# Performance work log

Hardware: AMD Instinct MI355X
Metric: run time of the kernel (lower is better)

## Reference

```python
import jax, jax.numpy as jnp
import numpy as np

TANH_SCALAR = 10.0  # taug in IrEne eq. 1 (close_to_one setting)

N_NODES = 2**21 - 1   # complete binary tree, depth D=21
N_LEAVES = 2**20
NUM_FEATURES = 64


def setup_inputs() -> dict:
    key = jax.random.key(0)
    k1, k2, k3, k4 = jax.random.split(key, 4)
    features = jax.random.normal(k1, (N_NODES, NUM_FEATURES), dtype=jnp.float32)
    leaf_energy = jax.random.uniform(k2, (N_LEAVES,), dtype=jnp.float32)
    W = jax.random.normal(k3, (NUM_FEATURES, 1), dtype=jnp.float32) * 0.1
    b = jax.random.normal(k4, (1,), dtype=jnp.float32) * 0.1
    return {"features": features, "leaf_energy": leaf_energy, "W": W, "b": b}


def reference(features, leaf_energy, W, b):
    """Batched equivalent of RecursiveTreeComputation (close_to_one, end2end).

    Tree layout: complete binary tree in level order; node i's parent is (i-1)//2.
    Level d occupies indices [2^d - 1, 2^{d+1} - 1). Leaves are the last level.
    parent_energy = sum_children score(child) * child_energy,
    score(f) = 1 + tanh(f @ W + b) / tanh_scalar.
    Returns predicted energy for every node, shape [N].
    """
    N, F = features.shape
    D = int(np.log2(N + 1))  # number of levels (static)

    # One fused pass over all nodes: Linear(F,1) + tanh + affine (WeightingModel).
    scores = 1.0 + jnp.tanh(features @ W + b)[:, 0] / TANH_SCALAR  # [N]

    leaf_start = 2 ** (D - 1) - 1
    energy = jnp.zeros((N,), dtype=features.dtype).at[leaf_start:].set(leaf_energy)

    # Level-wise bottom-up accumulation; consecutive child pairs share a parent.
    for d in range(D - 1, 0, -1):
        start, end = 2 ** d - 1, 2 ** (d + 1) - 1          # children at level d
        contrib = scores[start:end] * energy[start:end]      # weighted child energies
        parent_vals = contrib.reshape(-1, 2).sum(axis=1)     # sum sibling pairs
        pstart = 2 ** (d - 1) - 1                             # parents at level d-1
        energy = energy.at[pstart:start].set(energy[pstart:start] + parent_vals)
    return energy
```

## Files before the change

### kernel.cpp

```cpp
#include <hip/hip_runtime.h>
#include <cmath>

#define N_NODES_C   ((1 << 21) - 1)
#define N_LEAVES_C  (1 << 20)
#define LEAF_START  (N_LEAVES_C - 1)
#define NFEAT       64

__device__ __forceinline__ float score_fn(float dot, float bias) {
    return 1.0f + tanhf(dot + bias) * 0.1f;
}

__global__ __launch_bounds__(256) void scores_kernel(
        const float* __restrict__ features,
        const float* __restrict__ W,
        const float* __restrict__ b,
        float* __restrict__ scores) {
    const int q = threadIdx.x & 15;
    const float4 w4 = ((const float4*)W)[q];
    const float bias = b[0];
    const int group0 = (blockIdx.x * 256 + threadIdx.x) >> 4;
    const int stride = (gridDim.x * 256) >> 4;
    for (int node = group0; node < N_NODES_C; node += stride) {
        const float4 f = ((const float4*)(features + (size_t)node * NFEAT))[q];
        float v = f.x * w4.x + f.y * w4.y + f.z * w4.z + f.w * w4.w;
        v += __shfl_xor(v, 1);
        v += __shfl_xor(v, 2);
        v += __shfl_xor(v, 4);
        v += __shfl_xor(v, 8);
        if (q == 0) scores[node] = score_fn(v, bias);
    }
}

__global__ __launch_bounds__(256) void stage1_kernel(
        const float* __restrict__ scores,
        const float* __restrict__ leaf_energy,
        float* __restrict__ out) {
    __shared__ float buf[2][4096];
    const int blk = blockIdx.x;
    const int tid = threadIdx.x;
    const int leaf_off = blk * 4096;

    for (int i = tid; i < 4096; i += 256) {
        const int g = LEAF_START + leaf_off + i;
        const float e = leaf_energy[leaf_off + i];
        out[g] = e;
        buf[0][i] = scores[g] * e;
    }
    __syncthreads();

    int p = 0;
    for (int pd = 19; pd >= 8; --pd) {
        const int m = 1 << (pd - 8);
        const int base = (1 << pd) - 1 + blk * m;
        for (int j = tid; j < m; j += 256) {
            const float val = buf[p][2 * j] + buf[p][2 * j + 1];
            out[base + j] = val;
            buf[1 - p][j] = scores[base + j] * val;
        }
        p ^= 1;
        __syncthreads();
    }
}

__global__ __launch_bounds__(256) void stage2_kernel(
        const float* __restrict__ scores,
        float* __restrict__ out) {
    __shared__ float buf[2][256];
    const int tid = threadIdx.x;
    buf[0][tid] = scores[255 + tid] * out[255 + tid];
    __syncthreads();
    int p = 0;
    for (int pd = 7; pd >= 0; --pd) {
        const int m = 1 << pd;
        const int base = m - 1;
        if (tid < m) {
            const float val = buf[p][2 * tid] + buf[p][2 * tid + 1];
            out[base + tid] = val;
            buf[1 - p][tid] = scores[base + tid] * val;
        }
        p ^= 1;
        __syncthreads();
    }
}

extern "C" void kernel_launch(void* const* d_in, const int* in_sizes, int n_in,
                              void* d_out, int out_size, void* d_ws, size_t ws_size,
                              hipStream_t stream) {
    const float* features    = (const float*)d_in[0];
    const float* leaf_energy = (const float*)d_in[1];
    const float* W           = (const float*)d_in[2];
    const float* b           = (const float*)d_in[3];
    float* out    = (float*)d_out;
    float* scores = (float*)d_ws;

    scores_kernel<<<32768, 256, 0, stream>>>(features, W, b, scores);
    stage1_kernel<<<256, 256, 0, stream>>>(scores, leaf_energy, out);
    stage2_kernel<<<1, 256, 0, stream>>>(scores, out);
}
```

Measured before the change: 691.8 us.

## Fuse score computation into per-subtree tree reduction and a single top-level kernel

Removes the separate scores pass and its workspace array. Each of 2048 blocks now computes scores for its own 512-leaf subtree straight from the features and reduces it up to level 11 in shared memory. A single 1024-thread block then computes scores for the top 4095 nodes and finishes the reduction. This drops the global write and re-read of scores and one launch, and gives the reduction far more parallel blocks than the old 256-block stage. The cost is a serial single-block top kernel and less memory-level parallelism per block for the feature loads.

```diff
diff --git a/kernel.cpp b/kernel.cpp
--- a/kernel.cpp
+++ b/kernel.cpp
@@ -10,90 +10,115 @@
     return 1.0f + tanhf(dot + bias) * 0.1f;
 }
 
-__global__ __launch_bounds__(256) void scores_kernel(
+__device__ __forceinline__ float dot16(const float4 f, const float4 w) {
+    float v = f.x * w.x + f.y * w.y + f.z * w.z + f.w * w.w;
+    v += __shfl_xor(v, 1);
+    v += __shfl_xor(v, 2);
+    v += __shfl_xor(v, 4);
+    v += __shfl_xor(v, 8);
+    return v;
+}
+
+__global__ __launch_bounds__(256) void tree_reduce_kernel(
+        const float* __restrict__ features,
+        const float* __restrict__ leaf_energy,
+        const float* __restrict__ W,
+        const float* __restrict__ b,
+        float* __restrict__ out) {
+    __shared__ float sc[512];
+    __shared__ float buf[2][512];
+    const int tid = threadIdx.x;
+    const int q   = tid & 15;
+    const int grp = tid >> 4;
+    const int blk = blockIdx.x;
+    const float4 w4 = ((const float4*)W)[q];
+    const float bias = b[0];
+    const int l0 = blk << 9;
+
+    for (int i = tid; i < 512; i += 256)
+        out[LEAF_START + l0 + i] = leaf_energy[l0 + i];
+
+    for (int pd = 19; pd >= 12; --pd) {
+        const int m = 1 << (pd - 11);
+        const int gbase = ((1 << pd) - 1) + blk * m;
+        const int off = 512 - 2 * m;
+        for (int j = grp; j < m; j += 16) {
+            const float4 f = ((const float4*)(features + (size_t)(gbase + j) * NFEAT))[q];
+            const float v = dot16(f, w4);
+            if (q == 0) sc[off + j] = score_fn(v, bias);
+        }
+    }
+
+    for (int j = grp; j < 512; j += 16) {
+        const size_t g = (size_t)(LEAF_START + l0 + j);
+        const float4 f = ((const float4*)(features + g * NFEAT))[q];
+        const float v = dot16(f, w4);
+        if (q == 0) buf[0][j] = score_fn(v, bias) * leaf_energy[l0 + j];
+    }
+
+    int p = 0;
+    for (int pd = 19; pd >= 11; --pd) {
+        const int m = 1 << (pd - 11);
+        __syncthreads();
+        const int gbase = ((1 << pd) - 1) + blk * m;
+        for (int j = tid; j < m; j += 256) {
+            const float val = buf[p][2 * j] + buf[p][2 * j + 1];
+            out[gbase + j] = val;
+            if (pd > 11)
+                buf[1 - p][j] = sc[(512 - 2 * m) + j] * val;
+        }
+        p ^= 1;
+    }
+}
+
+__global__ __launch_bounds__(1024) void top_kernel(
         const float* __restrict__ features,
         const float* __restrict__ W,
         const float* __restrict__ b,
-        float* __restrict__ scores) {
-    const int q = threadIdx.x & 15;
+        float* __restrict__ out) {
+    __shared__ float slds[4096];
+    __shared__ float buf[2][2048];
+    const int tid = threadIdx.x;
+    const int q   = tid & 15;
+    const int grp = tid >> 4;
     const float4 w4 = ((const float4*)W)[q];
     const float bias = b[0];
-    const int group0 = (blockIdx.x * 256 + threadIdx.x) >> 4;
-    const int stride = (gridDim.x * 256) >> 4;
-    for (int node = group0; node < N_NODES_C; node += stride) {
-        const float4 f = ((const float4*)(features + (size_t)node * NFEAT))[q];
-        float v = f.x * w4.x + f.y * w4.y + f.z * w4.z + f.w * w4.w;
-        v += __shfl_xor(v, 1);
-        v += __shfl_xor(v, 2);
-        v += __shfl_xor(v, 4);
-        v += __shfl_xor(v, 8);
-        if (q == 0) scores[node] = score_fn(v, bias);
-    }
-}
 
-__global__ __launch_bounds__(256) void stage1_kernel(
-        const float* __restrict__ scores,
-        const float* __restrict__ leaf_energy,
-        float* __restrict__ out) {
-    __shared__ float buf[2][4096];
-    const int blk = blockIdx.x;
-    const int tid = threadIdx.x;
-    const int leaf_off = blk * 4096;
-
-    for (int i = tid; i < 4096; i += 256) {
-        const int g = LEAF_START + leaf_off + i;
-        const float e = leaf_energy[leaf_off + i];
-        out[g] = e;
-        buf[0][i] = scores[g] * e;
+    for (int j = grp; j < 4095; j += 64) {
+        const float4 f = ((const float4*)(features + (size_t)j * NFEAT))[q];
+        const float v = dot16(f, w4);
+        if (q == 0) slds[j] = score_fn(v, bias);
     }
     __syncthreads();
 
+    for (int i = tid; i < 2048; i += 1024)
+        buf[0][i] = slds[2047 + i] * out[2047 + i];
+
     int p = 0;
-    for (int pd = 19; pd >= 8; --pd) {
-        const int m = 1 << (pd - 8);
-        const int base = (1 << pd) - 1 + blk * m;
-        for (int j = tid; j < m; j += 256) {
+    for (int pd = 10; pd >= 0; --pd) {
+        const int m = 1 << pd;
+        __syncthreads();
+        const int base = m - 1;
+        for (int j = tid; j < m; j += 1024) {
             const float val = buf[p][2 * j] + buf[p][2 * j + 1];
             out[base + j] = val;
-            buf[1 - p][j] = scores[base + j] * val;
+            if (pd > 0)
+                buf[1 - p][j] = slds[base + j] * val;
         }
         p ^= 1;
-        __syncthreads();
-    }
-}
-
-__global__ __launch_bounds__(256) void stage2_kernel(
-        const float* __restrict__ scores,
-        float* __restrict__ out) {
-    __shared__ float buf[2][256];
-    const int tid = threadIdx.x;
-    buf[0][tid] = scores[255 + tid] * out[255 + tid];
-    __syncthreads();
-    int p = 0;
-    for (int pd = 7; pd >= 0; --pd) {
-        const int m = 1 << pd;
-        const int base = m - 1;
-        if (tid < m) {
-            const float val = buf[p][2 * tid] + buf[p][2 * tid + 1];
-            out[base + tid] = val;
-            buf[1 - p][tid] = scores[base + tid] * val;
-        }
-        p ^= 1;
-        __syncthreads();
     }
 }
 
 extern "C" void kernel_launch(void* const* d_in, const int* in_sizes, int n_in,
                               void* d_out, int out_size, void* d_ws, size_t ws_size,
                               hipStream_t stream) {
+    (void)in_sizes; (void)n_in; (void)out_size; (void)d_ws; (void)ws_size;
     const float* features    = (const float*)d_in[0];
     const float* leaf_energy = (const float*)d_in[1];
     const float* W           = (const float*)d_in[2];
     const float* b           = (const float*)d_in[3];
-    float* out    = (float*)d_out;
-    float* scores = (float*)d_ws;
+    float* out = (float*)d_out;
 
-    scores_kernel<<<32768, 256, 0, stream>>>(features, W, b, scores);
-    stage1_kernel<<<256, 256, 0, stream>>>(scores, leaf_energy, out);
-    stage2_kernel<<<1, 256, 0, stream>>>(scores, out);
+    tree_reduce_kernel<<<2048, 256, 0, stream>>>(features, leaf_energy, W, b, out);
+    top_kernel<<<1, 1024, 0, stream>>>(features, W, b, out);
 }
```

Measured after the change: 739.6 us. 1.07x slower.
